# Optimization experiments

Measured on AMD Instinct MI355X. Metric: run time of the kernel, lower is better.

Reference implementation:

```python
import jax, jax.numpy as jnp
import numpy as np

N, D_IN, UNITS = 8192, 4096, 4096

def setup_inputs() -> dict:
    key = jax.random.key(0)
    k1, k2 = jax.random.split(key)
    x = jax.random.normal(k1, (N, D_IN), dtype=jnp.float32)
    # weight initialized RandomNormal(stddev=0.1) in the original build()
    w = jax.random.normal(k2, (D_IN, UNITS), dtype=jnp.float32) * 0.1
    return {"x": x, "w": w}

def reference(x, w):
    # BinaryDense: sign-binarize both activations and weights, then dense matmul.
    # tf.sign semantics: sign(0) == 0, matched by jnp.sign.
    x_bin = jnp.sign(x)  # [N, d_in]
    w_bin = jnp.sign(w)  # [d_in, units]
    return jnp.matmul(x_bin, w_bin)  # [N, units]
```

## Files before the change

kernel.cpp:

```cpp
#include <hip/hip_runtime.h>
#include <stdint.h>

#define M_DIM 8192
#define K_DIM 4096
#define N_DIM 4096
#define KB (K_DIM / 2)

typedef unsigned char u8;
typedef unsigned int u32;
typedef int i32x4 __attribute__((ext_vector_type(4)));
typedef int i32x8 __attribute__((ext_vector_type(8)));
typedef float f32x4 __attribute__((ext_vector_type(4)));
typedef float float4v __attribute__((ext_vector_type(4)));
typedef u32 u32x2 __attribute__((ext_vector_type(2)));

__device__ __forceinline__ u32 sign_fp4(float v) {
  return v > 0.0f ? 0x2u : (v < 0.0f ? 0xAu : 0x0u);
}

__global__ void binarize_x_kernel(const float* __restrict__ in, u32* __restrict__ out, int n8) {
  int i = blockIdx.x * blockDim.x + threadIdx.x;
  int stride = gridDim.x * blockDim.x;
  for (; i < n8; i += stride) {
    float4v v0 = ((const float4v*)in)[2 * i];
    float4v v1 = ((const float4v*)in)[2 * i + 1];
    u32 w = sign_fp4(v0.x) | (sign_fp4(v0.y) << 4) | (sign_fp4(v0.z) << 8) |
            (sign_fp4(v0.w) << 12) | (sign_fp4(v1.x) << 16) | (sign_fp4(v1.y) << 20) |
            (sign_fp4(v1.z) << 24) | (sign_fp4(v1.w) << 28);
    out[i] = w;
  }
}

__global__ void binT_w_kernel(const float* __restrict__ w, u8* __restrict__ wT) {
  __shared__ u8 tile[64][65];
  const int bn = blockIdx.x * 64;
  const int bk = blockIdx.y * 64;
  const int tid = threadIdx.x;

#pragma unroll
  for (int it = 0; it < 4; ++it) {
    int idx = tid + it * 256;
    int r = idx >> 4;
    int c = (idx & 15) * 4;
    float4v v = *(const float4v*)&w[(size_t)(bk + r) * N_DIM + bn + c];
    tile[c + 0][r] = (u8)sign_fp4(v.x);
    tile[c + 1][r] = (u8)sign_fp4(v.y);
    tile[c + 2][r] = (u8)sign_fp4(v.z);
    tile[c + 3][r] = (u8)sign_fp4(v.w);
  }
  __syncthreads();
  const int rn = tid >> 2;
  const int cb = (tid & 3) * 8;
  u32x2 o;
  u32 lo = 0, hi = 0;
#pragma unroll
  for (int j = 0; j < 4; ++j) {
    lo |= (u32)(tile[rn][cb * 2 + 2 * j] | (tile[rn][cb * 2 + 2 * j + 1] << 4)) << (8 * j);
    hi |= (u32)(tile[rn][cb * 2 + 8 + 2 * j] | (tile[rn][cb * 2 + 9 + 2 * j] << 4)) << (8 * j);
  }
  o.x = lo;
  o.y = hi;
  *(u32x2*)&wT[(size_t)(bn + rn) * KB + (bk >> 1) + cb] = o;
}

#define BM 256
#define BN 256
#define BKB 128
#define NT (K_DIM / 256)

__device__ __forceinline__ void gload_lds16(const u8* g, u8* l) {
  __builtin_amdgcn_global_load_lds(
      (const __attribute__((address_space(1))) void*)g,
      (__attribute__((address_space(3))) void*)l, 16, 0, 0);
}

__device__ __forceinline__ i32x8 pad8(i32x4 v) {
  return __builtin_shufflevector(v, v, 0, 1, 2, 3, 0, 1, 2, 3);
}

__device__ __forceinline__ f32x4 mfma_fp4(i32x4 a, i32x4 b, f32x4 c) {
  return __builtin_amdgcn_mfma_scale_f32_16x16x128_f8f6f4(pad8(a), pad8(b), c, 4, 4, 0, 0x7F, 0,
                                                          0x7F);
}

__global__ __launch_bounds__(512, 2) void gemm_bin_fp4(const u8* __restrict__ A,
                                                       const u8* __restrict__ Bt,
                                                       float* __restrict__ C) {
  __shared__ u8 lds[2][4][128 * 128];

  const int tid = threadIdx.x;
  const int lane = tid & 63;
  const int wid = tid >> 6;
  const int wr = wid >> 2;
  const int wc = wid & 3;

  const int b = blockIdx.x;
  const int sw = (b & 7) * (gridDim.x >> 3) + (b >> 3);
  const int tiles_n = N_DIM / BN;
  const int bm = (sw / tiles_n) * BM;
  const int bn = (sw % tiles_n) * BN;

  const int l15 = lane & 15;
  const int g4 = lane >> 4;
  const int srow = lane >> 3;
  const int swz_src = (((lane & 7) ^ srow) << 4);

  auto stage = [&](int buf, int slot, const u8* gbase) {
#pragma unroll
    for (int i = 0; i < 2; ++i) {
      const u8* g = gbase + (size_t)(i * 64 + wid * 8 + srow) * KB + swz_src;
      gload_lds16(g, &lds[buf][slot][(i * 64 + wid * 8) * 128]);
    }
  };

  f32x4 acc[8][4] = {};

  {
    const u8* Abase = A + (size_t)bm * KB;
    const u8* Bbase = Bt + (size_t)bn * KB;
    stage(0, 0, Abase);
    stage(0, 1, Abase + (size_t)128 * KB);
    stage(0, 2, Bbase);
    stage(0, 3, Bbase + (size_t)128 * KB);
    stage(1, 2, Bbase + BKB);
    stage(1, 3, Bbase + (size_t)128 * KB + BKB);
  }
  asm volatile("s_waitcnt vmcnt(4)" ::: "memory");
  __builtin_amdgcn_s_barrier();

  i32x4 a[4][2], b01[2][2], b23[2][2];

  for (int t = 0; t < NT; ++t) {
    const int buf = t & 1;
    const u8* As = &lds[buf][wr][0];
    const u8* Bs = &lds[buf][2 + (wc >> 1)][0];
    const int brow0 = (wc & 1) * 64;
    const u8* Anext = A + (size_t)bm * KB + (t + 1) * BKB;
    const u8* Bnext2 = Bt + (size_t)bn * KB + (t + 2) * BKB;

#pragma unroll
    for (int m = 0; m < 4; ++m)
#pragma unroll
      for (int kk = 0; kk < 2; ++kk) {
        int row = m * 16 + l15;
        int col = (kk * 64 + g4 * 16) ^ ((row & 7) << 4);
        a[m][kk] = *(const i32x4*)&As[row * 128 + col];
      }
#pragma unroll
    for (int n = 0; n < 2; ++n)
#pragma unroll
      for (int kk = 0; kk < 2; ++kk) {
        int row = brow0 + n * 16 + l15;
        int col = (kk * 64 + g4 * 16) ^ ((row & 7) << 4);
        b01[n][kk] = *(const i32x4*)&Bs[row * 128 + col];
      }
    if (t + 1 < NT) stage(buf ^ 1, 0, Anext);
    __builtin_amdgcn_s_barrier();
    asm volatile("s_waitcnt lgkmcnt(0)" ::: "memory");
    __builtin_amdgcn_sched_barrier(0);
    __builtin_amdgcn_s_setprio(1);
#pragma unroll
    for (int kk = 0; kk < 2; ++kk)
#pragma unroll
      for (int m = 0; m < 4; ++m)
#pragma unroll
        for (int n = 0; n < 2; ++n)
          acc[m][n] = mfma_fp4(a[m][kk], b01[n][kk], acc[m][n]);
    __builtin_amdgcn_s_setprio(0);
    __builtin_amdgcn_s_barrier();

#pragma unroll
    for (int n = 0; n < 2; ++n)
#pragma unroll
      for (int kk = 0; kk < 2; ++kk) {
        int row = brow0 + (2 + n) * 16 + l15;
        int col = (kk * 64 + g4 * 16) ^ ((row & 7) << 4);
        b23[n][kk] = *(const i32x4*)&Bs[row * 128 + col];
      }
    if (t + 1 < NT) stage(buf ^ 1, 1, Anext + (size_t)128 * KB);
    __builtin_amdgcn_s_barrier();
    asm volatile("s_waitcnt lgkmcnt(0)" ::: "memory");
    __builtin_amdgcn_sched_barrier(0);
    __builtin_amdgcn_s_setprio(1);
#pragma unroll
    for (int kk = 0; kk < 2; ++kk)
#pragma unroll
      for (int m = 0; m < 4; ++m)
#pragma unroll
        for (int n = 0; n < 2; ++n)
          acc[m][2 + n] = mfma_fp4(a[m][kk], b23[n][kk], acc[m][2 + n]);
    __builtin_amdgcn_s_setprio(0);
    __builtin_amdgcn_s_barrier();

#pragma unroll
    for (int m = 0; m < 4; ++m)
#pragma unroll
      for (int kk = 0; kk < 2; ++kk) {
        int row = 64 + m * 16 + l15;
        int col = (kk * 64 + g4 * 16) ^ ((row & 7) << 4);
        a[m][kk] = *(const i32x4*)&As[row * 128 + col];
      }
    if (t + 2 < NT) stage(buf, 2, Bnext2);
    __builtin_amdgcn_s_barrier();
    asm volatile("s_waitcnt lgkmcnt(0)" ::: "memory");
    __builtin_amdgcn_sched_barrier(0);
    __builtin_amdgcn_s_setprio(1);
#pragma unroll
    for (int kk = 0; kk < 2; ++kk)
#pragma unroll
      for (int m = 0; m < 4; ++m)
#pragma unroll
        for (int n = 0; n < 2; ++n)
          acc[4 + m][n] = mfma_fp4(a[m][kk], b01[n][kk], acc[4 + m][n]);
    __builtin_amdgcn_s_setprio(0);
    __builtin_amdgcn_s_barrier();

    if (t + 2 < NT) stage(buf, 3, Bnext2 + (size_t)128 * KB);
    __builtin_amdgcn_s_barrier();
    __builtin_amdgcn_s_setprio(1);
#pragma unroll
    for (int kk = 0; kk < 2; ++kk)
#pragma unroll
      for (int m = 0; m < 4; ++m)
#pragma unroll
        for (int n = 0; n < 2; ++n)
          acc[4 + m][2 + n] = mfma_fp4(a[m][kk], b23[n][kk], acc[4 + m][2 + n]);
    __builtin_amdgcn_s_setprio(0);
    if (t + 2 < NT)
      asm volatile("s_waitcnt vmcnt(4)" ::: "memory");
    else
      asm volatile("s_waitcnt vmcnt(0)" ::: "memory");
    __builtin_amdgcn_s_barrier();
  }

  const int crow0 = bm + wr * 128;
  const int ccol0 = bn + wc * 64;
#pragma unroll
  for (int m = 0; m < 8; ++m)
#pragma unroll
    for (int n = 0; n < 4; ++n)
#pragma unroll
      for (int j = 0; j < 4; ++j)
        C[(size_t)(crow0 + m * 16 + g4 * 4 + j) * N_DIM + ccol0 + n * 16 + l15] = acc[m][n][j];
}

__global__ void naive_bin_gemm(const float* __restrict__ X, const float* __restrict__ W,
                               float* __restrict__ C) {
  int j = blockIdx.x * blockDim.x + threadIdx.x;
  int i = blockIdx.y;
  if (j >= N_DIM) return;
  float s = 0.0f;
  for (int k = 0; k < K_DIM; ++k) {
    float xv = X[(size_t)i * K_DIM + k];
    float wv = W[(size_t)k * N_DIM + j];
    float sx = (float)((xv > 0.0f) - (xv < 0.0f));
    float sw = (float)((wv > 0.0f) - (wv < 0.0f));
    s += sx * sw;
  }
  C[(size_t)i * N_DIM + j] = s;
}

extern "C" void kernel_launch(void* const* d_in, const int* in_sizes, int n_in,
                              void* d_out, int out_size, void* d_ws, size_t ws_size,
                              hipStream_t stream) {
  const float* x = (const float*)d_in[0];
  const float* w = (const float*)d_in[1];
  float* out = (float*)d_out;

  const size_t xb_bytes = (size_t)M_DIM * KB;
  const size_t wt_bytes = (size_t)N_DIM * KB;

  if (ws_size >= xb_bytes + wt_bytes) {
    u8* xb = (u8*)d_ws;
    u8* wt = (u8*)((char*)d_ws + xb_bytes);

    binarize_x_kernel<<<2048, 256, 0, stream>>>(x, (u32*)xb, M_DIM * K_DIM / 8);
    binT_w_kernel<<<dim3(N_DIM / 64, K_DIM / 64), dim3(256), 0, stream>>>(w, wt);

    const int grid = (M_DIM / BM) * (N_DIM / BN);
    gemm_bin_fp4<<<grid, 512, 0, stream>>>(xb, wt, out);
  } else {
    naive_bin_gemm<<<dim3(N_DIM / 256, M_DIM), dim3(256), 0, stream>>>(x, w, out);
  }
}
```

Baseline: 129.2 us.

## Switch FP4 GEMM inner loop from 16x16x128 to 32x32x64 scaled MFMA

Replaces the 16x16x128 scaled FP4 MFMA with the 32x32x64 variant. The warp tile is re-split into 2x2 blocks of 32x32 accumulators, and the LDS fragment loads and output store indexing change to match the new lane layout. The aim is fewer MFMA issues and fewer LDS fragment reads per unit of work, since the larger instruction reuses operands more. The cost is a different register layout and a more complex output store pattern, with some risk of mis-indexing.

```diff
diff --git a/kernel.cpp b/kernel.cpp
--- a/kernel.cpp
+++ b/kernel.cpp
@@ -10,7 +10,7 @@
 typedef unsigned int u32;
 typedef int i32x4 __attribute__((ext_vector_type(4)));
 typedef int i32x8 __attribute__((ext_vector_type(8)));
-typedef float f32x4 __attribute__((ext_vector_type(4)));
+typedef float f32x16 __attribute__((ext_vector_type(16)));
 typedef float float4v __attribute__((ext_vector_type(4)));
 typedef u32 u32x2 __attribute__((ext_vector_type(2)));
 
@@ -78,9 +78,8 @@
   return __builtin_shufflevector(v, v, 0, 1, 2, 3, 0, 1, 2, 3);
 }
 
-__device__ __forceinline__ f32x4 mfma_fp4(i32x4 a, i32x4 b, f32x4 c) {
-  return __builtin_amdgcn_mfma_scale_f32_16x16x128_f8f6f4(pad8(a), pad8(b), c, 4, 4, 0, 0x7F, 0,
-                                                          0x7F);
+__device__ __forceinline__ f32x16 mfma_fp4_32(i32x8 a, i32x8 b, f32x16 c) {
+  return __builtin_amdgcn_mfma_scale_f32_32x32x64_f8f6f4(a, b, c, 4, 4, 0, 0x7F, 0, 0x7F);
 }
 
 __global__ __launch_bounds__(512, 2) void gemm_bin_fp4(const u8* __restrict__ A,
@@ -100,8 +99,8 @@
   const int bm = (sw / tiles_n) * BM;
   const int bn = (sw % tiles_n) * BN;
 
-  const int l15 = lane & 15;
-  const int g4 = lane >> 4;
+  const int l31 = lane & 31;
+  const int g5 = lane >> 5;
   const int srow = lane >> 3;
   const int swz_src = (((lane & 7) ^ srow) << 4);
 
@@ -113,7 +112,7 @@
     }
   };
 
-  f32x4 acc[8][4] = {};
+  f32x16 acc[4][2] = {};
 
   {
     const u8* Abase = A + (size_t)bm * KB;
@@ -128,7 +127,7 @@
   asm volatile("s_waitcnt vmcnt(4)" ::: "memory");
   __builtin_amdgcn_s_barrier();
 
-  i32x4 a[4][2], b01[2][2], b23[2][2];
+  i32x4 a[2][4], b0[4], b1[4];
 
   for (int t = 0; t < NT; ++t) {
     const int buf = t & 1;
@@ -139,92 +138,100 @@
     const u8* Bnext2 = Bt + (size_t)bn * KB + (t + 2) * BKB;
 
 #pragma unroll
-    for (int m = 0; m < 4; ++m)
-#pragma unroll
-      for (int kk = 0; kk < 2; ++kk) {
-        int row = m * 16 + l15;
-        int col = (kk * 64 + g4 * 16) ^ ((row & 7) << 4);
-        a[m][kk] = *(const i32x4*)&As[row * 128 + col];
+    for (int m = 0; m < 2; ++m)
+#pragma unroll
+      for (int ks = 0; ks < 4; ++ks) {
+        int row = m * 32 + l31;
+        int col = (ks * 32 + g5 * 16) ^ ((row & 7) << 4);
+        a[m][ks] = *(const i32x4*)&As[row * 128 + col];
       }
 #pragma unroll
-    for (int n = 0; n < 2; ++n)
-#pragma unroll
-      for (int kk = 0; kk < 2; ++kk) {
-        int row = brow0 + n * 16 + l15;
-        int col = (kk * 64 + g4 * 16) ^ ((row & 7) << 4);
-        b01[n][kk] = *(const i32x4*)&Bs[row * 128 + col];
-      }
+    for (int ks = 0; ks < 4; ++ks) {
+      int row = brow0 + l31;
+      int col = (ks * 32 + g5 * 16) ^ ((row & 7) << 4);
+      b0[ks] = *(const i32x4*)&Bs[row * 128 + col];
+    }
     if (t + 1 < NT) stage(buf ^ 1, 0, Anext);
     __builtin_amdgcn_s_barrier();
     asm volatile("s_waitcnt lgkmcnt(0)" ::: "memory");
     __builtin_amdgcn_sched_barrier(0);
     __builtin_amdgcn_s_setprio(1);
-#pragma unroll
-    for (int kk = 0; kk < 2; ++kk)
-#pragma unroll
-      for (int m = 0; m < 4; ++m)
-#pragma unroll
-        for (int n = 0; n < 2; ++n)
-          acc[m][n] = mfma_fp4(a[m][kk], b01[n][kk], acc[m][n]);
-    __builtin_amdgcn_s_setprio(0);
-    __builtin_amdgcn_s_barrier();
-
-#pragma unroll
-    for (int n = 0; n < 2; ++n)
-#pragma unroll
-      for (int kk = 0; kk < 2; ++kk) {
-        int row = brow0 + (2 + n) * 16 + l15;
-        int col = (kk * 64 + g4 * 16) ^ ((row & 7) << 4);
-        b23[n][kk] = *(const i32x4*)&Bs[row * 128 + col];
-      }
+    {
+      i32x8 pb[4];
+#pragma unroll
+      for (int ks = 0; ks < 4; ++ks) pb[ks] = pad8(b0[ks]);
+#pragma unroll
+      for (int ks = 0; ks < 4; ++ks)
+#pragma unroll
+        for (int m = 0; m < 2; ++m)
+          acc[m][0] = mfma_fp4_32(pad8(a[m][ks]), pb[ks], acc[m][0]);
+    }
+    __builtin_amdgcn_s_setprio(0);
+    __builtin_amdgcn_s_barrier();
+
+#pragma unroll
+    for (int ks = 0; ks < 4; ++ks) {
+      int row = brow0 + 32 + l31;
+      int col = (ks * 32 + g5 * 16) ^ ((row & 7) << 4);
+      b1[ks] = *(const i32x4*)&Bs[row * 128 + col];
+    }
     if (t + 1 < NT) stage(buf ^ 1, 1, Anext + (size_t)128 * KB);
     __builtin_amdgcn_s_barrier();
     asm volatile("s_waitcnt lgkmcnt(0)" ::: "memory");
     __builtin_amdgcn_sched_barrier(0);
     __builtin_amdgcn_s_setprio(1);
-#pragma unroll
-    for (int kk = 0; kk < 2; ++kk)
-#pragma unroll
-      for (int m = 0; m < 4; ++m)
-#pragma unroll
-        for (int n = 0; n < 2; ++n)
-          acc[m][2 + n] = mfma_fp4(a[m][kk], b23[n][kk], acc[m][2 + n]);
-    __builtin_amdgcn_s_setprio(0);
-    __builtin_amdgcn_s_barrier();
-
-#pragma unroll
-    for (int m = 0; m < 4; ++m)
-#pragma unroll
-      for (int kk = 0; kk < 2; ++kk) {
-        int row = 64 + m * 16 + l15;
-        int col = (kk * 64 + g4 * 16) ^ ((row & 7) << 4);
-        a[m][kk] = *(const i32x4*)&As[row * 128 + col];
+    {
+      i32x8 pb[4];
+#pragma unroll
+      for (int ks = 0; ks < 4; ++ks) pb[ks] = pad8(b1[ks]);
+#pragma unroll
+      for (int ks = 0; ks < 4; ++ks)
+#pragma unroll
+        for (int m = 0; m < 2; ++m)
+          acc[m][1] = mfma_fp4_32(pad8(a[m][ks]), pb[ks], acc[m][1]);
+    }
+    __builtin_amdgcn_s_setprio(0);
+    __builtin_amdgcn_s_barrier();
+
+#pragma unroll
+    for (int m = 0; m < 2; ++m)
+#pragma unroll
+      for (int ks = 0; ks < 4; ++ks) {
+        int row = 64 + m * 32 + l31;
+        int col = (ks * 32 + g5 * 16) ^ ((row & 7) << 4);
+        a[m][ks] = *(const i32x4*)&As[row * 128 + col];
       }
     if (t + 2 < NT) stage(buf, 2, Bnext2);
     __builtin_amdgcn_s_barrier();
     asm volatile("s_waitcnt lgkmcnt(0)" ::: "memory");
     __builtin_amdgcn_sched_barrier(0);
     __builtin_amdgcn_s_setprio(1);
-#pragma unroll
-    for (int kk = 0; kk < 2; ++kk)
-#pragma unroll
-      for (int m = 0; m < 4; ++m)
-#pragma unroll
-        for (int n = 0; n < 2; ++n)
-          acc[4 + m][n] = mfma_fp4(a[m][kk], b01[n][kk], acc[4 + m][n]);
+    {
+      i32x8 pb[4];
+#pragma unroll
+      for (int ks = 0; ks < 4; ++ks) pb[ks] = pad8(b0[ks]);
+#pragma unroll
+      for (int ks = 0; ks < 4; ++ks)
+#pragma unroll
+        for (int m = 0; m < 2; ++m)
+          acc[2 + m][0] = mfma_fp4_32(pad8(a[m][ks]), pb[ks], acc[2 + m][0]);
+    }
     __builtin_amdgcn_s_setprio(0);
     __builtin_amdgcn_s_barrier();
 
     if (t + 2 < NT) stage(buf, 3, Bnext2 + (size_t)128 * KB);
     __builtin_amdgcn_s_barrier();
     __builtin_amdgcn_s_setprio(1);
-#pragma unroll
-    for (int kk = 0; kk < 2; ++kk)
-#pragma unroll
-      for (int m = 0; m < 4; ++m)
-#pragma unroll
-        for (int n = 0; n < 2; ++n)
-          acc[4 + m][2 + n] = mfma_fp4(a[m][kk], b23[n][kk], acc[4 + m][2 + n]);
+    {
+      i32x8 pb[4];
+#pragma unroll
+      for (int ks = 0; ks < 4; ++ks) pb[ks] = pad8(b1[ks]);
+#pragma unroll
+      for (int ks = 0; ks < 4; ++ks)
+#pragma unroll
+        for (int m = 0; m < 2; ++m)
+          acc[2 + m][1] = mfma_fp4_32(pad8(a[m][ks]), pb[ks], acc[2 + m][1]);
+    }
     __builtin_amdgcn_s_setprio(0);
     if (t + 2 < NT)
       asm volatile("s_waitcnt vmcnt(4)" ::: "memory");
@@ -236,12 +243,14 @@
   const int crow0 = bm + wr * 128;
   const int ccol0 = bn + wc * 64;
 #pragma unroll
-  for (int m = 0; m < 8; ++m)
-#pragma unroll
-    for (int n = 0; n < 4; ++n)
-#pragma unroll
-      for (int j = 0; j < 4; ++j)
-        C[(size_t)(crow0 + m * 16 + g4 * 4 + j) * N_DIM + ccol0 + n * 16 + l15] = acc[m][n][j];
+  for (int mt = 0; mt < 4; ++mt)
+#pragma unroll
+    for (int nt = 0; nt < 2; ++nt)
+#pragma unroll
+      for (int j = 0; j < 16; ++j) {
+        int row = crow0 + mt * 32 + (j & 3) + 8 * (j >> 2) + 4 * g5;
+        C[(size_t)row * N_DIM + ccol0 + nt * 32 + l31] = acc[mt][nt][j];
+      }
 }
 
 __global__ void naive_bin_gemm(const float* __restrict__ X, const float* __restrict__ W,
```

Measured after the change: 133.6 us. +3.4%, slower.
